# Kernel tuning notes

Hardware: AMD Instinct MI355X
Metric: run time of the kernel (lower is better)

The kernel has to match this reference:

```python
import jax, jax.numpy as jnp
import numpy as np

IN_DIM = 256   # opt.word_vec_size
MEM_DIM = 256  # opt.rnn_size // num_directions
N_LEAVES = 131072  # 2**17, complete binary tree


def setup_inputs() -> dict:
    key = jax.random.key(0)
    ks = jax.random.split(key, 8)
    s = 0.05  # weight scale
    return {
        # leaf word2vec embeddings, in-order leaf sequence of the tree
        "x": jax.random.normal(ks[0], (N_LEAVES, IN_DIM), jnp.float32),
        # BinaryTreeLeafModule params (Linear as x @ W + b)
        "Wcx": jax.random.normal(ks[1], (IN_DIM, MEM_DIM), jnp.float32) * s,
        "bcx": jnp.zeros((MEM_DIM,), jnp.float32),
        "Wox": jax.random.normal(ks[2], (IN_DIM, MEM_DIM), jnp.float32) * s,
        "box": jnp.zeros((MEM_DIM,), jnp.float32),
        # BinaryTreeComposer params: 4 left-child gates (i, lf, rf, u) fused
        # along the output dim, likewise 4 right-child gates.
        "Wl": jax.random.normal(ks[3], (MEM_DIM, 4 * MEM_DIM), jnp.float32) * s,
        "bl": jnp.zeros((4 * MEM_DIM,), jnp.float32),
        "Wr": jax.random.normal(ks[4], (MEM_DIM, 4 * MEM_DIM), jnp.float32) * s,
        "br": jnp.zeros((4 * MEM_DIM,), jnp.float32),
        "lengths": N_LEAVES,  # max sequence length for output padding
    }


def reference(x, Wcx, bcx, Wox, box, Wl, bl, Wr, br, lengths):
    m = Wcx.shape[1]
    # ---- BinaryTreeLeafModule, batched over all leaves ----
    c = x @ Wcx + bcx                                   # [n, m]
    h = jax.nn.sigmoid(x @ Wox + box) * jnp.tanh(c)     # [n, m]
    leaf_h = h  # in-order cat of leaf outputs == recursive cat([lo, ro])

    # ---- BinaryTreeComposer, one batched step per tree level ----
    # Loop over log2(n_leaves) levels of a complete binary tree; each
    # iteration composes adjacent sibling pairs (shapes static -> jit-safe).
    while c.shape[0] > 1:
        lc, rc = c[0::2], c[1::2]
        lh, rh = h[0::2], h[1::2]
        g = (lh @ Wl + bl) + (rh @ Wr + br)             # [n/2, 4m]
        gi, glf, grf, gu = jnp.split(g, 4, axis=-1)
        i = jax.nn.sigmoid(gi)
        lf = jax.nn.sigmoid(glf)
        rf = jax.nn.sigmoid(grf)
        u = jnp.tanh(gu)
        c = i * u + lf * lc + rf * rc                   # [n/2, m]
        h = jnp.tanh(c)                                 # gate_output=False

    # ---- root post-processing (as in original when tree.parent is None) ----
    output = leaf_h[:, None, :]                         # [n_leaves, 1, m]
    supl = int(lengths) - output.shape[0]
    if supl > 0:
        output = jnp.concatenate(
            [output, jnp.zeros((supl, 1, m), output.dtype)], axis=0)
    c_root = c[:, None, :]                              # [1, 1, m]
    h_root = h[:, None, :]                              # [1, 1, m]
    return output, (c_root, h_root)
```

## Files before the change

### kernel.cpp

```cpp
#include <hip/hip_runtime.h>
#include <cstdint>
#include <cstddef>


typedef float floatx4 __attribute__((ext_vector_type(4)));
typedef __bf16 bf16x8 __attribute__((ext_vector_type(8)));

typedef __attribute__((address_space(1))) unsigned int u32g;
typedef __attribute__((address_space(3))) unsigned int u32l;

__device__ __forceinline__ void async_copy16(const void* g, void* l) {
  __builtin_amdgcn_global_load_lds((u32g*)(uintptr_t)g, (u32l*)l, 16, 0, 0);
}

__device__ __forceinline__ float sigf(float x) {
  return 1.f / (1.f + __expf(-x));
}
__device__ __forceinline__ float tanh_f(float x) {
  x = fminf(fmaxf(x, -15.f), 15.f);
  float e = __expf(2.f * x);
  return (e - 1.f) / (e + 1.f);
}

__global__ void prep_leaf(const float* __restrict__ Wcx, const float* __restrict__ bcx,
                          const float* __restrict__ Wox, const float* __restrict__ box,
                          __bf16* __restrict__ WleafT, float* __restrict__ bleaf) {
  int n = blockIdx.x;
  int k = threadIdx.x;
  const float* src = (n < 256) ? Wcx : Wox;
  int col = n & 255;
  WleafT[n * 256 + k] = (__bf16)src[k * 256 + col];
  if (k == 0) bleaf[n] = (n < 256) ? bcx[col] : box[col];
}

__global__ void prep_cat(const float* __restrict__ Wl, const float* __restrict__ bl,
                         const float* __restrict__ Wr, const float* __restrict__ br,
                         __bf16* __restrict__ WcatT, float* __restrict__ bcat) {
  int n = blockIdx.x;
  for (int k = threadIdx.x; k < 512; k += 256) {
    const float* src = (k < 256) ? Wl : Wr;
    WcatT[n * 512 + k] = (__bf16)src[(size_t)(k & 255) * 1024 + n];
  }
  if (threadIdx.x == 0) bcat[n] = bl[n] + br[n];
}

__global__ __launch_bounds__(256, 4) void leaf_kernel(
    const float* __restrict__ x,
    const __bf16* __restrict__ WT,
    const float* __restrict__ bleaf,
    __bf16* __restrict__ c_out,
    __bf16* __restrict__ h_out,
    float* __restrict__ h_out32)
{
  __shared__ __bf16 SMEM[16384];
  const int tid  = threadIdx.x;
  const int wave = tid >> 6;
  const int lane = tid & 63;
  const int quad = lane >> 4;
  const int l15  = lane & 15;

  const int lid = blockIdx.y * gridDim.x + blockIdx.x;
  const int nwg = gridDim.x * gridDim.y;
  const int swz = (lid & 7) * (nwg >> 3) + (lid >> 3);
  const int j0  = (swz & 3) * 64;
  const int bm  = swz >> 2;

  floatx4 acc[2][8];
#pragma unroll
  for (int r = 0; r < 2; ++r)
#pragma unroll
    for (int f = 0; f < 8; ++f) acc[r][f] = (floatx4){0.f, 0.f, 0.f, 0.f};

  for (int kk = 0; kk < 256; kk += 64) {
#pragma unroll
    for (int it = 0; it < 4; ++it) {
      int f = it * 256 + tid;
      int row = f >> 3, cc = f & 7;
      int cb = cc ^ (row & 7);
      const float4* gx = (const float4*)(x + (size_t)(bm * 128 + row) * 256 + kk + cc * 8);
      float4 u = gx[0], v = gx[1];
      bf16x8 a8 = {(__bf16)u.x, (__bf16)u.y, (__bf16)u.z, (__bf16)u.w,
                   (__bf16)v.x, (__bf16)v.y, (__bf16)v.z, (__bf16)v.w};
      *(bf16x8*)&SMEM[row * 64 + cb * 8] = a8;
      int ng = ((row >> 6) << 8) + j0 + (row & 63);
      async_copy16(WT + (size_t)ng * 256 + kk + cb * 8, &SMEM[8192 + (f & ~63) * 8]);
    }
    __syncthreads();
#pragma unroll
    for (int s = 0; s < 2; ++s) {
      const int b  = (s * 4 + quad) ^ (l15 & 7);
      const int kb = b * 8;
      bf16x8 a0 = *(const bf16x8*)&SMEM[(wave * 32 + l15) * 64 + kb];
      bf16x8 a1 = *(const bf16x8*)&SMEM[(wave * 32 + 16 + l15) * 64 + kb];
#pragma unroll
      for (int f = 0; f < 8; ++f) {
        bf16x8 b8 = *(const bf16x8*)&SMEM[8192 + (f * 16 + l15) * 64 + kb];
        acc[0][f] = __builtin_amdgcn_mfma_f32_16x16x32_bf16(a0, b8, acc[0][f], 0, 0, 0);
        acc[1][f] = __builtin_amdgcn_mfma_f32_16x16x32_bf16(a1, b8, acc[1][f], 0, 0, 0);
      }
    }
    __syncthreads();
  }

  const int R0 = bm * 128;
#pragma unroll
  for (int r = 0; r < 2; ++r) {
#pragma unroll
    for (int q = 0; q < 4; ++q) {
      int col = j0 + q * 16 + l15;
      float bC = bleaf[col];
      float bO = bleaf[256 + col];
#pragma unroll
      for (int reg = 0; reg < 4; ++reg) {
        int lr = wave * 32 + r * 16 + quad * 4 + reg;
        int lc = q * 16 + l15;
        float c = acc[r][q][reg] + bC;
        float o = acc[r][q + 4][reg] + bO;
        float h = sigf(o) * tanh_f(c);
        h_out32[(size_t)(R0 + lr) * 256 + col] = h;
        int ch  = (lc >> 3) ^ ((lr ^ (lr >> 3)) & 7);
        int idx = lr * 64 + ch * 8 + (lc & 7);
        SMEM[idx]        = (__bf16)c;
        SMEM[8192 + idx] = (__bf16)h;
      }
    }
  }
  __syncthreads();
#pragma unroll
  for (int i = 0; i < 4; ++i) {
    int unit = i * 256 + tid;
    int lr = unit >> 3, k = unit & 7;
    int ch = k ^ ((lr ^ (lr >> 3)) & 7);
    bf16x8 vc = *(const bf16x8*)&SMEM[lr * 64 + ch * 8];
    bf16x8 vh = *(const bf16x8*)&SMEM[8192 + lr * 64 + ch * 8];
    size_t g = (size_t)(R0 + lr) * 256 + j0 + k * 8;
    *(bf16x8*)&c_out[g] = vc;
    *(bf16x8*)&h_out[g] = vh;
  }
}

template <typename OUT>
__global__ __launch_bounds__(256, 4) void tree_level(
    const __bf16* __restrict__ h_in,
    const __bf16* __restrict__ c_in,
    const __bf16* __restrict__ WT,
    const float* __restrict__ bcat,
    OUT* __restrict__ c_out,
    OUT* __restrict__ h_out,
    const int M)
{
  __shared__ __bf16 SMEM[16384];
  const int tid  = threadIdx.x;
  const int wave = tid >> 6;
  const int lane = tid & 63;
  const int quad = lane >> 4;
  const int l15  = lane & 15;

  const int lid = blockIdx.y * gridDim.x + blockIdx.x;
  const int nwg = gridDim.x * gridDim.y;
  const int swz = (lid & 7) * (nwg >> 3) + (lid >> 3);
  const int j0  = (swz & 7) * 32;
  const int bm  = swz >> 3;

  floatx4 acc[2][8];
#pragma unroll
  for (int r = 0; r < 2; ++r)
#pragma unroll
    for (int f = 0; f < 8; ++f) acc[r][f] = (floatx4){0.f, 0.f, 0.f, 0.f};

  for (int kk = 0; kk < 512; kk += 64) {
#pragma unroll
    for (int it = 0; it < 4; ++it) {
      int f = it * 256 + tid;
      int row = f >> 3, cc = f & 7;
      int cb = cc ^ (row & 7);
      int rg = bm * 128 + row;
      rg = rg < M ? rg : M - 1;
      async_copy16(h_in + (size_t)rg * 512 + kk + cb * 8, &SMEM[(f & ~63) * 8]);
      int ng = ((row >> 5) << 8) + j0 + (row & 31);
      async_copy16(WT + (size_t)ng * 512 + kk + cb * 8, &SMEM[8192 + (f & ~63) * 8]);
    }
    __syncthreads();
#pragma unroll
    for (int s = 0; s < 2; ++s) {
      const int b  = (s * 4 + quad) ^ (l15 & 7);
      const int kb = b * 8;
      bf16x8 a0 = *(const bf16x8*)&SMEM[(wave * 32 + l15) * 64 + kb];
      bf16x8 a1 = *(const bf16x8*)&SMEM[(wave * 32 + 16 + l15) * 64 + kb];
#pragma unroll
      for (int f = 0; f < 8; ++f) {
        bf16x8 b8 = *(const bf16x8*)&SMEM[8192 + (f * 16 + l15) * 64 + kb];
        acc[0][f] = __builtin_amdgcn_mfma_f32_16x16x32_bf16(a0, b8, acc[0][f], 0, 0, 0);
        acc[1][f] = __builtin_amdgcn_mfma_f32_16x16x32_bf16(a1, b8, acc[1][f], 0, 0, 0);
      }
    }
    __syncthreads();
  }

  if constexpr (sizeof(OUT) == 2) {
#pragma unroll
    for (int r = 0; r < 2; ++r) {
#pragma unroll
      for (int q = 0; q < 2; ++q) {
        int col = j0 + q * 16 + l15;
        float bi  = bcat[col];
        float blf = bcat[256 + col];
        float brf = bcat[512 + col];
        float bu  = bcat[768 + col];
#pragma unroll
        for (int reg = 0; reg < 4; ++reg) {
          int row = bm * 128 + wave * 32 + r * 16 + quad * 4 + reg;
          float cn = 0.f, hn = 0.f;
          if (row < M) {
            float lc = (float)c_in[(size_t)(2 * row) * 256 + col];
            float rc = (float)c_in[(size_t)(2 * row + 1) * 256 + col];
            float iv = sigf(acc[r][0 + q][reg] + bi);
            float lf = sigf(acc[r][2 + q][reg] + blf);
            float rf = sigf(acc[r][4 + q][reg] + brf);
            float uv = tanh_f(acc[r][6 + q][reg] + bu);
            cn = iv * uv + lf * lc + rf * rc;
            hn = tanh_f(cn);
          }
          int lr  = wave * 32 + r * 16 + quad * 4 + reg;
          int lcc = q * 16 + l15;
          int ch  = (lcc >> 3) ^ ((lr ^ (lr >> 2)) & 3);
          int idx = lr * 32 + ch * 8 + (lcc & 7);
          SMEM[idx]        = (__bf16)cn;
          SMEM[4096 + idx] = (__bf16)hn;
        }
      }
    }
    __syncthreads();
#pragma unroll
    for (int i = 0; i < 2; ++i) {
      int unit = i * 256 + tid;
      int lr = unit >> 2, k = unit & 3;
      int gr = bm * 128 + lr;
      if (gr < M) {
        int ch = k ^ ((lr ^ (lr >> 2)) & 3);
        bf16x8 vc = *(const bf16x8*)&SMEM[lr * 32 + ch * 8];
        bf16x8 vh = *(const bf16x8*)&SMEM[4096 + lr * 32 + ch * 8];
        size_t g = (size_t)gr * 256 + j0 + k * 8;
        *(bf16x8*)((__bf16*)c_out + g) = vc;
        *(bf16x8*)((__bf16*)h_out + g) = vh;
      }
    }
  } else {
#pragma unroll
    for (int r = 0; r < 2; ++r) {
#pragma unroll
      for (int q = 0; q < 2; ++q) {
        int col = j0 + q * 16 + l15;
        float bi  = bcat[col];
        float blf = bcat[256 + col];
        float brf = bcat[512 + col];
        float bu  = bcat[768 + col];
#pragma unroll
        for (int reg = 0; reg < 4; ++reg) {
          int row = bm * 128 + wave * 32 + r * 16 + quad * 4 + reg;
          if (row < M) {
            float lc = (float)c_in[(size_t)(2 * row) * 256 + col];
            float rc = (float)c_in[(size_t)(2 * row + 1) * 256 + col];
            float iv = sigf(acc[r][0 + q][reg] + bi);
            float lf = sigf(acc[r][2 + q][reg] + blf);
            float rf = sigf(acc[r][4 + q][reg] + brf);
            float uv = tanh_f(acc[r][6 + q][reg] + bu);
            float cn = iv * uv + lf * lc + rf * rc;
            float hn = tanh_f(cn);
            size_t idx = (size_t)row * 256 + col;
            c_out[idx] = (OUT)cn;
            h_out[idx] = (OUT)hn;
          }
        }
      }
    }
  }
}

extern "C" void kernel_launch(void* const* d_in, const int* in_sizes, int n_in,
                              void* d_out, int out_size, void* d_ws, size_t ws_size,
                              hipStream_t stream) {
  const float* x   = (const float*)d_in[0];
  const float* Wcx = (const float*)d_in[1];
  const float* bcx = (const float*)d_in[2];
  const float* Wox = (const float*)d_in[3];
  const float* box = (const float*)d_in[4];
  const float* Wl  = (const float*)d_in[5];
  const float* bl  = (const float*)d_in[6];
  const float* Wr  = (const float*)d_in[7];
  const float* br  = (const float*)d_in[8];

  const size_t LEAF = (size_t)131072 * 256;
  const size_t MiB  = 1ull << 20;
  char* ws = (char*)d_ws;

  __bf16* WleafT = (__bf16*)(ws);
  __bf16* WcatT  = (__bf16*)(ws + 262144);
  float*  bleaf  = (float*)(ws + 262144 + 1048576);
  float*  bcat   = bleaf + 512;

  int slog = 17;
  size_t ra_sz = 0, rb_sz = 0;
  while (slog > 11) {
    size_t SL  = (size_t)1 << slog;
    size_t nsl = (size_t)(131072 >> slog);
    ra_sz = SL * 512 > nsl * 524288 ? SL * 512 : nsl * 524288;
    rb_sz = SL * 256 > nsl * 262144 ? SL * 256 : nsl * 262144;
    size_t need = 2 * MiB + SL * 1024 + ra_sz + rb_sz + nsl * MiB;
    if (need <= ws_size) break;
    --slog;
  }
  const int SLAB  = 1 << slog;
  const int nslab = 131072 >> slog;

  char*   dyn = ws + 2 * MiB;
  __bf16* LC  = (__bf16*)dyn;
  __bf16* LH  = LC + (size_t)SLAB * 256;
  char*   RA  = (char*)(LH + (size_t)SLAB * 256);
  char*   RB  = RA + ra_sz;
  __bf16* CC  = (__bf16*)(RB + rb_sz);
  __bf16* CH  = CC + (size_t)nslab * 1024 * 256;

  float* out    = (float*)d_out;
  float* leaf_h = out;
  float* c_root = out + LEAF;
  float* h_root = out + LEAF + 256;

  prep_leaf<<<dim3(512), dim3(256), 0, stream>>>(Wcx, bcx, Wox, box, WleafT, bleaf);
  prep_cat<<<dim3(1024), dim3(256), 0, stream>>>(Wl, bl, Wr, br, WcatT, bcat);

  const int STOP = slog - 10;
  for (int sl = 0; sl < nslab; ++sl) {
    const size_t R0 = (size_t)sl * SLAB;
    leaf_kernel<<<dim3(4, SLAB / 128), dim3(256), 0, stream>>>(
        x + R0 * 256, WleafT, bleaf, LC, LH, leaf_h + R0 * 256);

    const __bf16* hin = LH;
    const __bf16* cin = LC;
    for (int lvl = 1; lvl <= STOP; ++lvl) {
      const int M = SLAB >> lvl;
      dim3 grid(8, (M + 127) / 128);
      __bf16 *cdst, *hdst;
      if (lvl == STOP) {
        cdst = CC + (size_t)sl * 1024 * 256;
        hdst = CH + (size_t)sl * 1024 * 256;
      } else {
        cdst = (__bf16*)((lvl & 1) ? RA : RB);
        hdst = cdst + (size_t)M * 256;
      }
      tree_level<__bf16><<<grid, dim3(256), 0, stream>>>(
          hin, cin, WcatT, bcat, cdst, hdst, M);
      hin = hdst; cin = cdst;
    }
  }

  {
    const __bf16* hin = CH;
    const __bf16* cin = CC;
    int pp = 1;
    for (int M = (nslab << 10) >> 1; M >= 1; M >>= 1, pp ^= 1) {
      dim3 grid(8, (M + 127) / 128);
      if (M == 1) {
        tree_level<float><<<grid, dim3(256), 0, stream>>>(
            hin, cin, WcatT, bcat, c_root, h_root, 1);
      } else {
        __bf16* cdst = (__bf16*)(pp ? RA : RB);
        __bf16* hdst = cdst + (size_t)M * 256;
        tree_level<__bf16><<<grid, dim3(256), 0, stream>>>(
            hin, cin, WcatT, bcat, cdst, hdst, M);
        hin = hdst; cin = cdst;
      }
    }
  }
}
```

Baseline: 715.5 us.

## Fuse small tree levels into one cooperative persistent kernel with grid sync

When the whole tree fits in one slab, the leaf pass and the large levels run as separate launches as before. All levels from M=8192 down to the root now run inside a single cooperative kernel that uses grid.sync between levels. This removes the launch overhead and idle tails of many small level kernels. The cost is grid-wide barriers, a grid of 512 blocks that must be co-resident, and a fallback path that launches per level if the cooperative launch fails.

After: 1.922 ms. 2.69x slower.

```diff
diff --git a/kernel.cpp b/kernel.cpp
--- a/kernel.cpp
+++ b/kernel.cpp
@@ -1,6 +1,9 @@
 #include <hip/hip_runtime.h>
+#include <hip/hip_cooperative_groups.h>
 #include <cstdint>
 #include <cstddef>
+
+namespace cg = cooperative_groups;
 
 
 typedef float floatx4 __attribute__((ext_vector_type(4)));
@@ -140,27 +143,20 @@
 }
 
 template <typename OUT>
-__global__ __launch_bounds__(256, 4) void tree_level(
+__device__ __forceinline__ void tree_body(
+    __bf16* SMEM,
     const __bf16* __restrict__ h_in,
     const __bf16* __restrict__ c_in,
     const __bf16* __restrict__ WT,
     const float* __restrict__ bcat,
     OUT* __restrict__ c_out,
     OUT* __restrict__ h_out,
-    const int M)
+    const int M, const int bm, const int j0, const int tid)
 {
-  __shared__ __bf16 SMEM[16384];
-  const int tid  = threadIdx.x;
   const int wave = tid >> 6;
   const int lane = tid & 63;
   const int quad = lane >> 4;
   const int l15  = lane & 15;
-
-  const int lid = blockIdx.y * gridDim.x + blockIdx.x;
-  const int nwg = gridDim.x * gridDim.y;
-  const int swz = (lid & 7) * (nwg >> 3) + (lid >> 3);
-  const int j0  = (swz & 7) * 32;
-  const int bm  = swz >> 3;
 
   floatx4 acc[2][8];
 #pragma unroll
@@ -277,6 +273,53 @@
   }
 }
 
+template <typename OUT>
+__global__ __launch_bounds__(256, 4) void tree_level(
+    const __bf16* __restrict__ h_in, const __bf16* __restrict__ c_in,
+    const __bf16* __restrict__ WT, const float* __restrict__ bcat,
+    OUT* __restrict__ c_out, OUT* __restrict__ h_out, const int M)
+{
+  __shared__ __bf16 SMEM[16384];
+  const int lid = blockIdx.y * gridDim.x + blockIdx.x;
+  const int nwg = gridDim.x * gridDim.y;
+  const int swz = (lid & 7) * (nwg >> 3) + (lid >> 3);
+  tree_body<OUT>(SMEM, h_in, c_in, WT, bcat, c_out, h_out,
+                 M, swz >> 3, (swz & 7) * 32, threadIdx.x);
+}
+
+__global__ __launch_bounds__(256, 2) void tree_tail(
+    const __bf16* h0, const __bf16* c0,
+    const __bf16* __restrict__ WT, const float* __restrict__ bcat,
+    __bf16* bufX, __bf16* bufY,
+    float* c_root, float* h_root, const int M0)
+{
+  cg::grid_group grid = cg::this_grid();
+  __shared__ __bf16 SMEM[16384];
+  const int tid  = threadIdx.x;
+  const int flat = blockIdx.y * gridDim.x + blockIdx.x;
+
+  const __bf16* hin = h0;
+  const __bf16* cin = c0;
+  int ping = 0;
+  for (int M = M0; M >= 2; M >>= 1, ping ^= 1) {
+    __bf16* cdst = ping ? bufY : bufX;
+    __bf16* hdst = cdst + (size_t)M * 256;
+    const int actn = 8 * ((M + 127) >> 7);
+    if (flat < actn) {
+      const int swz = (flat & 7) * (actn >> 3) + (flat >> 3);
+      tree_body<__bf16>(SMEM, hin, cin, WT, bcat, cdst, hdst,
+                        M, swz >> 3, (swz & 7) * 32, tid);
+    }
+    hin = hdst; cin = cdst;
+    __threadfence();
+    grid.sync();
+  }
+  if (flat < 8) {
+    tree_body<float>(SMEM, hin, cin, WT, bcat, c_root, h_root,
+                     1, 0, flat * 32, tid);
+  }
+}
+
 extern "C" void kernel_launch(void* const* d_in, const int* in_sizes, int n_in,
                               void* d_out, int out_size, void* d_ws, size_t ws_size,
                               hipStream_t stream) {
@@ -329,47 +372,87 @@
   prep_leaf<<<dim3(512), dim3(256), 0, stream>>>(Wcx, bcx, Wox, box, WleafT, bleaf);
   prep_cat<<<dim3(1024), dim3(256), 0, stream>>>(Wl, bl, Wr, br, WcatT, bcat);
 
-  const int STOP = slog - 10;
-  for (int sl = 0; sl < nslab; ++sl) {
-    const size_t R0 = (size_t)sl * SLAB;
+  if (nslab == 1) {
     leaf_kernel<<<dim3(4, SLAB / 128), dim3(256), 0, stream>>>(
-        x + R0 * 256, WleafT, bleaf, LC, LH, leaf_h + R0 * 256);
+        x, WleafT, bleaf, LC, LH, leaf_h);
 
     const __bf16* hin = LH;
     const __bf16* cin = LC;
-    for (int lvl = 1; lvl <= STOP; ++lvl) {
-      const int M = SLAB >> lvl;
-      dim3 grid(8, (M + 127) / 128);
-      __bf16 *cdst, *hdst;
-      if (lvl == STOP) {
-        cdst = CC + (size_t)sl * 1024 * 256;
-        hdst = CH + (size_t)sl * 1024 * 256;
-      } else {
-        cdst = (__bf16*)((lvl & 1) ? RA : RB);
-        hdst = cdst + (size_t)M * 256;
-      }
-      tree_level<__bf16><<<grid, dim3(256), 0, stream>>>(
+    int ping = 0;
+    int M = SLAB >> 1;
+    const int M0 = 8192;
+    while (M > M0) {
+      __bf16* cdst = (__bf16*)(ping ? RB : RA);
+      __bf16* hdst = cdst + (size_t)M * 256;
+      tree_level<__bf16><<<dim3(8, (M + 127) / 128), dim3(256), 0, stream>>>(
           hin, cin, WcatT, bcat, cdst, hdst, M);
-      hin = hdst; cin = cdst;
-    }
-  }
-
-  {
-    const __bf16* hin = CH;
-    const __bf16* cin = CC;
-    int pp = 1;
-    for (int M = (nslab << 10) >> 1; M >= 1; M >>= 1, pp ^= 1) {
-      dim3 grid(8, (M + 127) / 128);
-      if (M == 1) {
-        tree_level<float><<<grid, dim3(256), 0, stream>>>(
-            hin, cin, WcatT, bcat, c_root, h_root, 1);
-      } else {
-        __bf16* cdst = (__bf16*)(pp ? RA : RB);
-        __bf16* hdst = cdst + (size_t)M * 256;
+      hin = hdst; cin = cdst; ping ^= 1; M >>= 1;
+    }
+    __bf16* bufX = (__bf16*)(ping ? RB : RA);
+    __bf16* bufY = (__bf16*)(ping ? RA : RB);
+    void* kargs[] = {(void*)&hin, (void*)&cin, (void*)&WcatT, (void*)&bcat,
+                     (void*)&bufX, (void*)&bufY, (void*)&c_root, (void*)&h_root,
+                     (void*)&M};
+    hipError_t e = hipLaunchCooperativeKernel(
+        reinterpret_cast<void*>(tree_tail), dim3(8, M / 128), dim3(256),
+        kargs, 0, stream);
+    if (e != hipSuccess) {
+      while (M >= 1) {
+        if (M == 1) {
+          tree_level<float><<<dim3(8, 1), dim3(256), 0, stream>>>(
+              hin, cin, WcatT, bcat, c_root, h_root, 1);
+        } else {
+          __bf16* cdst = (__bf16*)(ping ? RB : RA);
+          __bf16* hdst = cdst + (size_t)M * 256;
+          tree_level<__bf16><<<dim3(8, (M + 127) / 128), dim3(256), 0, stream>>>(
+              hin, cin, WcatT, bcat, cdst, hdst, M);
+          hin = hdst; cin = cdst; ping ^= 1;
+        }
+        M >>= 1;
+      }
+    }
+  } else {
+    const int STOP = slog - 10;
+    for (int sl = 0; sl < nslab; ++sl) {
+      const size_t R0 = (size_t)sl * SLAB;
+      leaf_kernel<<<dim3(4, SLAB / 128), dim3(256), 0, stream>>>(
+          x + R0 * 256, WleafT, bleaf, LC, LH, leaf_h + R0 * 256);
+
+      const __bf16* hin = LH;
+      const __bf16* cin = LC;
+      for (int lvl = 1; lvl <= STOP; ++lvl) {
+        const int M = SLAB >> lvl;
+        dim3 grid(8, (M + 127) / 128);
+        __bf16 *cdst, *hdst;
+        if (lvl == STOP) {
+          cdst = CC + (size_t)sl * 1024 * 256;
+          hdst = CH + (size_t)sl * 1024 * 256;
+        } else {
+          cdst = (__bf16*)((lvl & 1) ? RA : RB);
+          hdst = cdst + (size_t)M * 256;
+        }
         tree_level<__bf16><<<grid, dim3(256), 0, stream>>>(
             hin, cin, WcatT, bcat, cdst, hdst, M);
         hin = hdst; cin = cdst;
       }
     }
-  }
-}
+    {
+      const __bf16* hin = CH;
+      const __bf16* cin = CC;
+      int pp = 1;
+      for (int M = (nslab << 10) >> 1; M >= 1; M >>= 1, pp ^= 1) {
+        dim3 grid(8, (M + 127) / 128);
+        if (M == 1) {
+          tree_level<float><<<grid, dim3(256), 0, stream>>>(
+              hin, cin, WcatT, bcat, c_root, h_root, 1);
+        } else {
+          __bf16* cdst = (__bf16*)(pp ? RA : RB);
+          __bf16* hdst = cdst + (size_t)M * 256;
+          tree_level<__bf16><<<grid, dim3(256), 0, stream>>>(
+              hin, cin, WcatT, bcat, cdst, hdst, M);
+          hin = hdst; cin = cdst;
+        }
+      }
+    }
+  }
+}
```

## Stage child cell states in LDS, cheaper activations, single-slab path

Applied to the files above, without the earlier changes.

The tree-level epilogue now copies the 256 child c rows for each block's column slice into LDS with async global-to-LDS copies, instead of issuing strided scalar global loads per element. Sigmoid and tanh use reciprocal-based formulas without clamping, which cuts divides but may lose some accuracy near saturation. A new single-slab path runs every level in one chain, skipping the intermediate CC/CH staging and the second reduction phase. The async copy reuses the B-tile region of LDS after the main loop and adds an extra barrier.

Measured after the change: 711.5 us. No clear change (-0.6%).

```diff
diff --git a/kernel.cpp b/kernel.cpp
--- a/kernel.cpp
+++ b/kernel.cpp
@@ -14,12 +14,11 @@
 }
 
 __device__ __forceinline__ float sigf(float x) {
-  return 1.f / (1.f + __expf(-x));
+  return __frcp_rn(1.f + __expf(-x));
 }
 __device__ __forceinline__ float tanh_f(float x) {
-  x = fminf(fmaxf(x, -15.f), 15.f);
-  float e = __expf(2.f * x);
-  return (e - 1.f) / (e + 1.f);
+  float e = __expf(-2.f * x);
+  return __builtin_fmaf(2.f, __frcp_rn(1.f + e), -1.f);
 }
 
 __global__ void prep_leaf(const float* __restrict__ Wcx, const float* __restrict__ bcx,
@@ -197,6 +196,20 @@
     __syncthreads();
   }
 
+  {
+    const int maxr = 2 * M - 1;
+#pragma unroll
+    for (int i = 0; i < 4; ++i) {
+      int chunk = i * 256 + tid;
+      int row = chunk >> 2, piece = chunk & 3;
+      int gr = bm * 256 + row;
+      gr = gr < maxr ? gr : maxr;
+      async_copy16(c_in + (size_t)gr * 256 + j0 + piece * 8,
+                   &SMEM[8192 + (chunk & ~63) * 8]);
+    }
+  }
+  __syncthreads();
+
   if constexpr (sizeof(OUT) == 2) {
 #pragma unroll
     for (int r = 0; r < 2; ++r) {
@@ -209,11 +222,13 @@
         float bu  = bcat[768 + col];
 #pragma unroll
         for (int reg = 0; reg < 4; ++reg) {
-          int row = bm * 128 + wave * 32 + r * 16 + quad * 4 + reg;
+          int lr  = wave * 32 + r * 16 + quad * 4 + reg;
+          int lcc = q * 16 + l15;
+          int row = bm * 128 + lr;
           float cn = 0.f, hn = 0.f;
           if (row < M) {
-            float lc = (float)c_in[(size_t)(2 * row) * 256 + col];
-            float rc = (float)c_in[(size_t)(2 * row + 1) * 256 + col];
+            float lc = (float)SMEM[8192 + (2 * lr) * 32 + lcc];
+            float rc = (float)SMEM[8192 + (2 * lr + 1) * 32 + lcc];
             float iv = sigf(acc[r][0 + q][reg] + bi);
             float lf = sigf(acc[r][2 + q][reg] + blf);
             float rf = sigf(acc[r][4 + q][reg] + brf);
@@ -221,8 +236,6 @@
             cn = iv * uv + lf * lc + rf * rc;
             hn = tanh_f(cn);
           }
-          int lr  = wave * 32 + r * 16 + quad * 4 + reg;
-          int lcc = q * 16 + l15;
           int ch  = (lcc >> 3) ^ ((lr ^ (lr >> 2)) & 3);
           int idx = lr * 32 + ch * 8 + (lcc & 7);
           SMEM[idx]        = (__bf16)cn;
@@ -257,10 +270,12 @@
         float bu  = bcat[768 + col];
 #pragma unroll
         for (int reg = 0; reg < 4; ++reg) {
-          int row = bm * 128 + wave * 32 + r * 16 + quad * 4 + reg;
+          int lr  = wave * 32 + r * 16 + quad * 4 + reg;
+          int lcc = q * 16 + l15;
+          int row = bm * 128 + lr;
           if (row < M) {
-            float lc = (float)c_in[(size_t)(2 * row) * 256 + col];
-            float rc = (float)c_in[(size_t)(2 * row + 1) * 256 + col];
+            float lc = (float)SMEM[8192 + (2 * lr) * 32 + lcc];
+            float rc = (float)SMEM[8192 + (2 * lr + 1) * 32 + lcc];
             float iv = sigf(acc[r][0 + q][reg] + bi);
             float lf = sigf(acc[r][2 + q][reg] + blf);
             float rf = sigf(acc[r][4 + q][reg] + brf);
@@ -329,47 +344,68 @@
   prep_leaf<<<dim3(512), dim3(256), 0, stream>>>(Wcx, bcx, Wox, box, WleafT, bleaf);
   prep_cat<<<dim3(1024), dim3(256), 0, stream>>>(Wl, bl, Wr, br, WcatT, bcat);
 
-  const int STOP = slog - 10;
-  for (int sl = 0; sl < nslab; ++sl) {
-    const size_t R0 = (size_t)sl * SLAB;
+  if (nslab == 1) {
     leaf_kernel<<<dim3(4, SLAB / 128), dim3(256), 0, stream>>>(
-        x + R0 * 256, WleafT, bleaf, LC, LH, leaf_h + R0 * 256);
+        x, WleafT, bleaf, LC, LH, leaf_h);
 
     const __bf16* hin = LH;
     const __bf16* cin = LC;
-    for (int lvl = 1; lvl <= STOP; ++lvl) {
+    for (int lvl = 1; lvl <= slog; ++lvl) {
       const int M = SLAB >> lvl;
       dim3 grid(8, (M + 127) / 128);
-      __bf16 *cdst, *hdst;
-      if (lvl == STOP) {
-        cdst = CC + (size_t)sl * 1024 * 256;
-        hdst = CH + (size_t)sl * 1024 * 256;
+      if (lvl == slog) {
+        tree_level<float><<<grid, dim3(256), 0, stream>>>(
+            hin, cin, WcatT, bcat, c_root, h_root, M);
       } else {
-        cdst = (__bf16*)((lvl & 1) ? RA : RB);
-        hdst = cdst + (size_t)M * 256;
-      }
-      tree_level<__bf16><<<grid, dim3(256), 0, stream>>>(
-          hin, cin, WcatT, bcat, cdst, hdst, M);
-      hin = hdst; cin = cdst;
-    }
-  }
-
-  {
-    const __bf16* hin = CH;
-    const __bf16* cin = CC;
-    int pp = 1;
-    for (int M = (nslab << 10) >> 1; M >= 1; M >>= 1, pp ^= 1) {
-      dim3 grid(8, (M + 127) / 128);
-      if (M == 1) {
-        tree_level<float><<<grid, dim3(256), 0, stream>>>(
-            hin, cin, WcatT, bcat, c_root, h_root, 1);
-      } else {
-        __bf16* cdst = (__bf16*)(pp ? RA : RB);
+        __bf16* cdst = (__bf16*)((lvl & 1) ? RA : RB);
         __bf16* hdst = cdst + (size_t)M * 256;
         tree_level<__bf16><<<grid, dim3(256), 0, stream>>>(
             hin, cin, WcatT, bcat, cdst, hdst, M);
         hin = hdst; cin = cdst;
       }
     }
-  }
-}
+  } else {
+    const int STOP = slog - 10;
+    for (int sl = 0; sl < nslab; ++sl) {
+      const size_t R0 = (size_t)sl * SLAB;
+      leaf_kernel<<<dim3(4, SLAB / 128), dim3(256), 0, stream>>>(
+          x + R0 * 256, WleafT, bleaf, LC, LH, leaf_h + R0 * 256);
+
+      const __bf16* hin = LH;
+      const __bf16* cin = LC;
+      for (int lvl = 1; lvl <= STOP; ++lvl) {
+        const int M = SLAB >> lvl;
+        dim3 grid(8, (M + 127) / 128);
+        __bf16 *cdst, *hdst;
+        if (lvl == STOP) {
+          cdst = CC + (size_t)sl * 1024 * 256;
+          hdst = CH + (size_t)sl * 1024 * 256;
+        } else {
+          cdst = (__bf16*)((lvl & 1) ? RA : RB);
+          hdst = cdst + (size_t)M * 256;
+        }
+        tree_level<__bf16><<<grid, dim3(256), 0, stream>>>(
+            hin, cin, WcatT, bcat, cdst, hdst, M);
+        hin = hdst; cin = cdst;
+      }
+    }
+    {
+      const __bf16* hin = CH;
+      const __bf16* cin = CC;
+      int pp = 1;
+      for (int M = (nslab << 10) >> 1; M >= 1; M >>= 1, pp ^= 1) {
+        dim3 grid(8, (M + 127) / 128);
+        if (M == 1) {
+          tree_level<float><<<grid, dim3(256), 0, stream>>>(
+              hin, cin, WcatT, bcat, c_root, h_root, 1);
+        } else {
+          __bf16* cdst = (__bf16*)(pp ? RA : RB);
+          __bf16* hdst = cdst + (size_t)M * 256;
+          tree_level<__bf16><<<grid, dim3(256), 0, stream>>>(
+              hin, cin, WcatT, bcat, cdst, hdst, M);
+          hin = hdst; cin = cdst;
+        }
+      }
+    }
+  }
+}
```
